# Performance work log

Hardware: AMD Instinct MI355X
Metric: run time of the kernel (lower is better)

Reference implementation:

```python
import jax, jax.numpy as jnp
import numpy as np
from itertools import combinations_with_replacement

INPUT_DIM = 128
DEGREE = 2

# Static index arrays for degree-2 terms (i<=j), matching
# combinations_with_replacement order.
_pairs = np.array(list(combinations_with_replacement(range(INPUT_DIM), DEGREE)), dtype=np.int32)
I_IDX = jnp.asarray(_pairs[:, 0])  # [d*(d+1)/2]
J_IDX = jnp.asarray(_pairs[:, 1])


def setup_inputs() -> dict:
    key = jax.random.key(0)
    k1, k2, k3 = jax.random.split(key, 3)
    B, D, N = 8192, INPUT_DIM, 512
    num_outputs = D + D * (D + 1) // 2  # 8384
    x = jax.random.normal(k1, (B, D), dtype=jnp.float32)
    weights = jax.random.normal(k2, (N, num_outputs), dtype=jnp.float32)
    bias = jax.random.normal(k3, (N,), dtype=jnp.float32)
    return {"x": x, "weights": weights, "bias": bias}


def reference(x, weights, bias):
    # Polynomial feature expansion: [x, x_i * x_j for i<=j]
    poly = x[:, I_IDX] * x[:, J_IDX]          # [B, d*(d+1)/2]
    feats = jnp.concatenate([x, poly], axis=1)  # [B, num_outputs]
    # (output.unsqueeze(1) * weights.unsqueeze(0)).sum(-1) == feats @ weights.T
    return jnp.einsum('bo,no->bn', feats, weights) + bias
```

## Files before the change

kernel.cpp:

```cpp
#include <hip/hip_runtime.h>
#include <hip/hip_bf16.h>
#include <stdint.h>

#define D_IN   128
#define NPOLY  8256
#define KDIM   8384
#define B_ROWS 8192
#define N_COLS 512

#define TBL_OFF   0
#define TBL_BYTES (NPOLY * 4)
#define WBF_OFF   (TBL_OFF + TBL_BYTES)
#define WBF_BYTES ((size_t)N_COLS * KDIM * 2)
#define FEA_OFF   (WBF_OFF + WBF_BYTES)
#define FEA_BYTES ((size_t)B_ROWS * KDIM * 2)
#define WS_NEED   (FEA_OFF + FEA_BYTES)

typedef __attribute__((ext_vector_type(8))) short bf16x8_t;
typedef __attribute__((ext_vector_type(4))) float f32x4_t;

__device__ __forceinline__ uint16_t f2bf(float f) {
  union { float f; uint32_t u; } c; c.f = f;
  uint32_t u = c.u;
  uint32_t r = (u + 0x7fffu + ((u >> 16) & 1u)) >> 16;
  return (uint16_t)r;
}

__device__ __forceinline__ void async_load16(void* lds_dst, const void* g_src) {
  __builtin_amdgcn_global_load_lds(
      (const __attribute__((address_space(1))) void*)g_src,
      (__attribute__((address_space(3))) void*)lds_dst,
      16, 0, 0);
}

__global__ void build_table(uint32_t* __restrict__ tbl) {
  int p = blockIdx.x * 256 + threadIdx.x;
  if (p >= NPOLY) return;
  float t = 66049.0f - 8.0f * (float)p;
  int i = (int)((257.0f - sqrtf(t)) * 0.5f);
  if (i < 0) i = 0; if (i > 127) i = 127;
  while (i < 127 && ((i + 1) * (257 - (i + 1))) / 2 <= p) ++i;
  while (i > 0 && (i * (257 - i)) / 2 > p) --i;
  int j = i + (p - (i * (257 - i)) / 2);
  tbl[p] = ((uint32_t)i << 8) | (uint32_t)j;
}

__global__ void wconv(const float* __restrict__ w, uint16_t* __restrict__ wb) {
  int idx = blockIdx.x * 256 + threadIdx.x;
  if (idx < N_COLS * KDIM) wb[idx] = f2bf(w[idx]);
}

__global__ void feat_gen(const float* __restrict__ x, const uint32_t* __restrict__ tbl,
                         uint16_t* __restrict__ feats) {
  __shared__ float xs[D_IN];
  int b = blockIdx.x;
  int tid = threadIdx.x;
  const float* xr = x + (size_t)b * D_IN;
  if (tid < D_IN) xs[tid] = xr[tid];
  __syncthreads();
  uint16_t* fr = feats + (size_t)b * KDIM;
  if (tid < D_IN) fr[tid] = f2bf(xs[tid]);
  for (int p = tid; p < NPOLY; p += 256) {
    uint32_t t = tbl[p];
    float v = xs[t >> 8] * xs[t & 255u];
    fr[D_IN + p] = f2bf(v);
  }
}

__global__ void init_out(float* __restrict__ out, const float* __restrict__ bias) {
  int idx = blockIdx.x * 256 + threadIdx.x;
  out[idx] = bias[idx & (N_COLS - 1)];
}

#define BMT 128
#define BNT 128
#define BKT 64
#define KSTEPS 131
#define KCUT 66

__global__ __launch_bounds__(256, 2) void gemm_poly(
    const uint16_t* __restrict__ A,
    const uint16_t* __restrict__ W,
    float* __restrict__ out) {
  __shared__ __align__(16) uint16_t sA[BMT * BKT];
  __shared__ __align__(16) uint16_t sW[BNT * BKT];

  const int tid  = threadIdx.x;
  const int lane = tid & 63;
  const int wv   = tid >> 6;
  const int wr   = wv >> 1;
  const int wc   = wv & 1;
  const int hi   = lane >> 4;
  const int lr   = lane & 15;

  const int b0 = blockIdx.x * BMT;
  const int n0 = blockIdx.y * BNT;
  const int kt0 = (blockIdx.z == 0) ? 0 : KCUT;
  const int kt1 = (blockIdx.z == 0) ? KCUT : KSTEPS;

  int rowq[4], cbxq[4];
#pragma unroll
  for (int q = 0; q < 4; ++q) {
    int L = q * 4096 + tid * 16;
    int row = L >> 7;
    int cb  = L & 127;
    rowq[q] = row;
    cbxq[q] = cb ^ ((row & 7) << 4);
  }

  int offA[4][2], offW[4][2];
#pragma unroll
  for (int f = 0; f < 4; ++f) {
    int rowA = wr * 64 + f * 16 + lr;
    int rowW = wc * 64 + f * 16 + lr;
#pragma unroll
    for (int kh = 0; kh < 2; ++kh) {
      int kb = kh * 64 + hi * 16;
      offA[f][kh] = rowA * 128 + (kb ^ ((rowA & 7) << 4));
      offW[f][kh] = rowW * 128 + (kb ^ ((rowW & 7) << 4));
    }
  }

  f32x4_t acc[4][4];
#pragma unroll
  for (int mf = 0; mf < 4; ++mf)
#pragma unroll
    for (int nf = 0; nf < 4; ++nf) {
      f32x4_t z = {0.f, 0.f, 0.f, 0.f};
      acc[mf][nf] = z;
    }

  const char* Ab = (const char*)A;
  const char* Wb = (const char*)W;

#define STAGE(kt)                                                              \
  {                                                                            \
    _Pragma("unroll")                                                          \
    for (int q = 0; q < 4; ++q) {                                              \
      const char* srcA =                                                       \
          Ab + ((size_t)(b0 + rowq[q]) * KDIM + (kt) * BKT) * 2 + cbxq[q];     \
      async_load16((char*)sA + q * 4096 + tid * 16, srcA);                     \
    }                                                                          \
    _Pragma("unroll")                                                          \
    for (int q = 0; q < 4; ++q) {                                              \
      const char* srcW =                                                       \
          Wb + ((size_t)(n0 + rowq[q]) * KDIM + (kt) * BKT) * 2 + cbxq[q];     \
      async_load16((char*)sW + q * 4096 + tid * 16, srcW);                     \
    }                                                                          \
  }

  STAGE(kt0);
  for (int kt = kt0; kt < kt1; ++kt) {
    __syncthreads();
    bf16x8_t a[4][2], b[4][2];
#pragma unroll
    for (int mf = 0; mf < 4; ++mf)
#pragma unroll
      for (int kh = 0; kh < 2; ++kh)
        a[mf][kh] = *(const bf16x8_t*)((const char*)sA + offA[mf][kh]);
#pragma unroll
    for (int nf = 0; nf < 4; ++nf)
#pragma unroll
      for (int kh = 0; kh < 2; ++kh)
        b[nf][kh] = *(const bf16x8_t*)((const char*)sW + offW[nf][kh]);
#pragma unroll
    for (int mf = 0; mf < 4; ++mf)
#pragma unroll
      for (int nf = 0; nf < 4; ++nf) {
        acc[mf][nf] = __builtin_amdgcn_mfma_f32_16x16x32_bf16(
            a[mf][0], b[nf][0], acc[mf][nf], 0, 0, 0);
        acc[mf][nf] = __builtin_amdgcn_mfma_f32_16x16x32_bf16(
            a[mf][1], b[nf][1], acc[mf][nf], 0, 0, 0);
      }
    __syncthreads();
    if (kt + 1 < kt1) STAGE(kt + 1);
  }

#pragma unroll
  for (int mf = 0; mf < 4; ++mf) {
    int row = b0 + wr * 64 + mf * 16 + hi * 4;
#pragma unroll
    for (int nf = 0; nf < 4; ++nf) {
      int col = n0 + wc * 64 + nf * 16 + lr;
#pragma unroll
      for (int r = 0; r < 4; ++r) {
        atomicAdd(&out[(size_t)(row + r) * N_COLS + col], acc[mf][nf][r]);
      }
    }
  }
#undef STAGE
}

__global__ void naive_poly(const float* __restrict__ x, const float* __restrict__ w,
                           const float* __restrict__ bias, float* __restrict__ out) {
  size_t o = (size_t)blockIdx.x * 256 + threadIdx.x;
  if (o >= (size_t)B_ROWS * N_COLS) return;
  int n = (int)(o >> 13);
  int b = (int)(o & (B_ROWS - 1));
  const float* xr = x + (size_t)b * D_IN;
  const float* wr = w + (size_t)n * KDIM;
  float acc = bias[n];
  for (int k = 0; k < D_IN; ++k) acc += wr[k] * xr[k];
  int p = D_IN;
  for (int i = 0; i < D_IN; ++i) {
    float xi = xr[i];
    for (int j = i; j < D_IN; ++j) acc += wr[p++] * xi * xr[j];
  }
  out[(size_t)b * N_COLS + n] = acc;
}

extern "C" void kernel_launch(void* const* d_in, const int* in_sizes, int n_in,
                              void* d_out, int out_size, void* d_ws, size_t ws_size,
                              hipStream_t stream) {
  const float* x    = (const float*)d_in[0];
  const float* w    = (const float*)d_in[1];
  const float* bias = (const float*)d_in[2];
  float* out = (float*)d_out;

  if (ws_size < WS_NEED) {
    naive_poly<<<(B_ROWS * N_COLS) / 256, 256, 0, stream>>>(x, w, bias, out);
    return;
  }

  char* ws = (char*)d_ws;
  uint32_t* tbl = (uint32_t*)(ws + TBL_OFF);
  uint16_t* wb  = (uint16_t*)(ws + WBF_OFF);
  uint16_t* fe  = (uint16_t*)(ws + FEA_OFF);

  build_table<<<(NPOLY + 255) / 256, 256, 0, stream>>>(tbl);
  wconv<<<(N_COLS * KDIM + 255) / 256, 256, 0, stream>>>(w, wb);
  feat_gen<<<B_ROWS, 256, 0, stream>>>(x, tbl, fe);
  init_out<<<(B_ROWS * N_COLS) / 256, 256, 0, stream>>>(out, bias);
  gemm_poly<<<dim3(B_ROWS / BMT, N_COLS / BNT, 2), 256, 0, stream>>>(fe, wb, out);
}
```

Before: 210.7 us.

## Fuse table build, weight conversion, feature gen and bias init into one prep kernel

Replaces four preprocessing launches with one fused kernel whose blocks split into feature-generation, output-bias-init, and weight-conversion ranges. Feature generation now handles two rows per block. It computes (i,j) pairs on the fly instead of reading an index table, stages results in shared memory and writes them out as 16-byte vectors. Conversions use the hardware packed bf16 conversion instruction, and the bias init and weight conversion are vectorized. This removes launch overhead, table traffic and narrow 2-byte stores, at the cost of more shared memory per block and branchy index walking.

Result: faster. 200.6 us (-4.8%).

```diff
diff --git a/kernel.cpp b/kernel.cpp
--- a/kernel.cpp
+++ b/kernel.cpp
@@ -8,22 +8,21 @@
 #define B_ROWS 8192
 #define N_COLS 512
 
-#define TBL_OFF   0
-#define TBL_BYTES (NPOLY * 4)
-#define WBF_OFF   (TBL_OFF + TBL_BYTES)
+#define WBF_OFF   0
 #define WBF_BYTES ((size_t)N_COLS * KDIM * 2)
-#define FEA_OFF   (WBF_OFF + WBF_BYTES)
+#define FEA_OFF   WBF_BYTES
 #define FEA_BYTES ((size_t)B_ROWS * KDIM * 2)
 #define WS_NEED   (FEA_OFF + FEA_BYTES)
 
-typedef __attribute__((ext_vector_type(8))) short bf16x8_t;
-typedef __attribute__((ext_vector_type(4))) float f32x4_t;
-
-__device__ __forceinline__ uint16_t f2bf(float f) {
-  union { float f; uint32_t u; } c; c.f = f;
-  uint32_t u = c.u;
-  uint32_t r = (u + 0x7fffu + ((u >> 16) & 1u)) >> 16;
-  return (uint16_t)r;
+typedef __attribute__((ext_vector_type(8))) short    bf16x8_t;
+typedef __attribute__((ext_vector_type(8))) float    f32x8_t;
+typedef __attribute__((ext_vector_type(4))) float    f32x4_t;
+typedef __attribute__((ext_vector_type(4))) uint32_t u32x4_t;
+
+__device__ __forceinline__ uint32_t pk2(float lo, float hi) {
+  uint32_t r;
+  asm("v_cvt_pk_bf16_f32 %0, %1, %2" : "=v"(r) : "v"(lo), "v"(hi));
+  return r;
 }
 
 __device__ __forceinline__ void async_load16(void* lds_dst, const void* g_src) {
@@ -33,43 +32,79 @@
       16, 0, 0);
 }
 
-__global__ void build_table(uint32_t* __restrict__ tbl) {
-  int p = blockIdx.x * 256 + threadIdx.x;
-  if (p >= NPOLY) return;
-  float t = 66049.0f - 8.0f * (float)p;
-  int i = (int)((257.0f - sqrtf(t)) * 0.5f);
-  if (i < 0) i = 0; if (i > 127) i = 127;
-  while (i < 127 && ((i + 1) * (257 - (i + 1))) / 2 <= p) ++i;
-  while (i > 0 && (i * (257 - i)) / 2 > p) --i;
-  int j = i + (p - (i * (257 - i)) / 2);
-  tbl[p] = ((uint32_t)i << 8) | (uint32_t)j;
-}
-
-__global__ void wconv(const float* __restrict__ w, uint16_t* __restrict__ wb) {
-  int idx = blockIdx.x * 256 + threadIdx.x;
-  if (idx < N_COLS * KDIM) wb[idx] = f2bf(w[idx]);
-}
-
-__global__ void feat_gen(const float* __restrict__ x, const uint32_t* __restrict__ tbl,
-                         uint16_t* __restrict__ feats) {
-  __shared__ float xs[D_IN];
-  int b = blockIdx.x;
-  int tid = threadIdx.x;
-  const float* xr = x + (size_t)b * D_IN;
-  if (tid < D_IN) xs[tid] = xr[tid];
-  __syncthreads();
-  uint16_t* fr = feats + (size_t)b * KDIM;
-  if (tid < D_IN) fr[tid] = f2bf(xs[tid]);
-  for (int p = tid; p < NPOLY; p += 256) {
-    uint32_t t = tbl[p];
-    float v = xs[t >> 8] * xs[t & 255u];
-    fr[D_IN + p] = f2bf(v);
-  }
-}
-
-__global__ void init_out(float* __restrict__ out, const float* __restrict__ bias) {
-  int idx = blockIdx.x * 256 + threadIdx.x;
-  out[idx] = bias[idx & (N_COLS - 1)];
+#define NB_FEAT 4096
+#define NB_INIT 4096
+#define NB_WCNV 2096
+__global__ __launch_bounds__(256) void fused_prep(
+    const float* __restrict__ x, const float* __restrict__ w,
+    const float* __restrict__ bias, float* __restrict__ out,
+    uint16_t* __restrict__ wb, uint16_t* __restrict__ feats) {
+  __shared__ float xs[2][D_IN];
+  __shared__ __align__(16) uint16_t pr[2][KDIM];
+  const int blk = blockIdx.x;
+  const int tid = threadIdx.x;
+
+  if (blk < NB_FEAT) {
+    const int r0 = blk * 2;
+    xs[tid >> 7][tid & 127] = x[(size_t)r0 * D_IN + tid];
+    __syncthreads();
+    if (tid < 32) {
+      int row = tid >> 4, c8 = (tid & 15) * 8;
+      u32x4_t o;
+#pragma unroll
+      for (int h = 0; h < 4; ++h)
+        o[h] = pk2(xs[row][c8 + 2 * h], xs[row][c8 + 2 * h + 1]);
+      *(u32x4_t*)&pr[row][c8] = o;
+    }
+    for (int it = 0; it < 5; ++it) {
+      int g = tid + it * 256;
+      if (g >= NPOLY / 8) break;
+      int p0 = 8 * g;
+      float t = 66049.0f - 8.0f * (float)p0;
+      int i = (int)((257.0f - sqrtf(t)) * 0.5f);
+      while (i > 0 && (i * (257 - i)) / 2 > p0) --i;
+      while (i < 127 && ((i + 1) * (257 - (i + 1))) / 2 <= p0) ++i;
+      int j = i + (p0 - (i * (257 - i)) / 2);
+      float xi0 = xs[0][i], xi1 = xs[1][i];
+      float q0[8], q1[8];
+#pragma unroll
+      for (int e = 0; e < 8; ++e) {
+        q0[e] = xi0 * xs[0][j];
+        q1[e] = xi1 * xs[1][j];
+        if (e < 7) {
+          if (j == 127) { ++i; j = i; xi0 = xs[0][i]; xi1 = xs[1][i]; }
+          else ++j;
+        }
+      }
+      u32x4_t o0, o1;
+#pragma unroll
+      for (int h = 0; h < 4; ++h) {
+        o0[h] = pk2(q0[2 * h], q0[2 * h + 1]);
+        o1[h] = pk2(q1[2 * h], q1[2 * h + 1]);
+      }
+      *(u32x4_t*)&pr[0][D_IN + p0] = o0;
+      *(u32x4_t*)&pr[1][D_IN + p0] = o1;
+    }
+    __syncthreads();
+    uint16_t* d0 = feats + (size_t)r0 * KDIM;
+    for (int q = tid; q < 2 * (KDIM / 8); q += 256) {
+      int row = (q >= KDIM / 8);
+      int g = q - (row ? KDIM / 8 : 0);
+      *(bf16x8_t*)(d0 + (size_t)row * KDIM + g * 8) =
+          *(const bf16x8_t*)&pr[row][g * 8];
+    }
+  } else if (blk < NB_FEAT + NB_INIT) {
+    int idx = (blk - NB_FEAT) * 256 + tid;
+    f32x4_t bv = *(const f32x4_t*)(bias + ((idx * 4) & (N_COLS - 1)));
+    *(f32x4_t*)(out + (size_t)idx * 4) = bv;
+  } else {
+    int g = (blk - NB_FEAT - NB_INIT) * 256 + tid;
+    f32x8_t v = *(const f32x8_t*)(w + (size_t)g * 8);
+    u32x4_t o;
+#pragma unroll
+    for (int h = 0; h < 4; ++h) o[h] = pk2(v[2 * h], v[2 * h + 1]);
+    *(u32x4_t*)(wb + (size_t)g * 8) = o;
+  }
 }
 
 #define BMT 128
@@ -223,13 +258,9 @@
   }
 
   char* ws = (char*)d_ws;
-  uint32_t* tbl = (uint32_t*)(ws + TBL_OFF);
   uint16_t* wb  = (uint16_t*)(ws + WBF_OFF);
   uint16_t* fe  = (uint16_t*)(ws + FEA_OFF);
 
-  build_table<<<(NPOLY + 255) / 256, 256, 0, stream>>>(tbl);
-  wconv<<<(N_COLS * KDIM + 255) / 256, 256, 0, stream>>>(w, wb);
-  feat_gen<<<B_ROWS, 256, 0, stream>>>(x, tbl, fe);
-  init_out<<<(B_ROWS * N_COLS) / 256, 256, 0, stream>>>(out, bias);
+  fused_prep<<<NB_FEAT + NB_INIT + NB_WCNV, 256, 0, stream>>>(x, w, bias, out, wb, fe);
   gemm_poly<<<dim3(B_ROWS / BMT, N_COLS / BNT, 2), 256, 0, stream>>>(fe, wb, out);
 }
```
